# Performance work log

Hardware: AMD Instinct MI355X
Metric: run time of the kernel (lower is better)

## Reference

```python
import jax, jax.numpy as jnp
import numpy as np

B, T, D, H = 8, 1024, 768, 12
HD = D // H  # 64
EPS = 1e-5


def setup_inputs() -> dict:
    key = jax.random.key(0)
    ks = jax.random.split(key, 16)
    s = lambda fan_in: 1.0 / np.sqrt(fan_in)
    inp = {
        "x": jax.random.normal(ks[0], (B, T, D), jnp.float32),
        # per-head Q/K/V projections stacked: [H, D, HD]
        "wq": jax.random.normal(ks[1], (H, D, HD), jnp.float32) * s(D),
        "bq": jnp.zeros((H, HD), jnp.float32),
        "wk": jax.random.normal(ks[2], (H, D, HD), jnp.float32) * s(D),
        "bk": jnp.zeros((H, HD), jnp.float32),
        "wv": jax.random.normal(ks[3], (H, D, HD), jnp.float32) * s(D),
        "bv": jnp.zeros((H, HD), jnp.float32),
        "w_proj": jax.random.normal(ks[4], (D, D), jnp.float32) * s(D),
        "b_proj": jnp.zeros((D,), jnp.float32),
        "g1": jnp.ones((D,), jnp.float32),
        "be1": jnp.zeros((D,), jnp.float32),
        "g2": jnp.ones((D,), jnp.float32),
        "be2": jnp.zeros((D,), jnp.float32),
        "w_fc": jax.random.normal(ks[5], (D, 4 * D), jnp.float32) * s(D),
        "b_fc": jnp.zeros((4 * D,), jnp.float32),
        "w_cp": jax.random.normal(ks[6], (4 * D, D), jnp.float32) * s(4 * D),
        "b_cp": jnp.zeros((D,), jnp.float32),
    }
    return inp


def _layernorm(x, g, b):
    mu = jnp.mean(x, axis=-1, keepdims=True)
    var = jnp.var(x, axis=-1, keepdims=True)
    return (x - mu) * jax.lax.rsqrt(var + EPS) * g + b


def _block(x, wq, bq, wk, bk, wv, bv, w_proj, b_proj, g1, be1, g2, be2,
           w_fc, b_fc, w_cp, b_cp):
    # --- attention sublayer ---
    h = _layernorm(x, g1, be1)
    q = jnp.einsum('btd,hdk->bhtk', h, wq) + bq[None, :, None, :]
    k = jnp.einsum('btd,hdk->bhtk', h, wk) + bk[None, :, None, :]
    v = jnp.einsum('btd,hdk->bhtk', h, wv) + bv[None, :, None, :]
    scale = 1.0 / np.sqrt(HD)
    scores = jnp.einsum('bhqk,bhtk->bhqt', q, k) * scale  # [B,H,T,T]
    causal = jnp.tril(jnp.ones((T, T), bool))
    scores = jnp.where(causal, scores, jnp.finfo(scores.dtype).min)
    attn = jax.nn.softmax(scores, axis=-1)
    y = jnp.einsum('bhqt,bhtk->bhqk', attn, v)           # [B,H,T,HD]
    y = y.transpose(0, 2, 1, 3).reshape(x.shape[0], x.shape[1], D)
    x = x + y @ w_proj + b_proj
    # --- MLP sublayer ---
    h2 = _layernorm(x, g2, be2)
    h2 = jax.nn.gelu(h2 @ w_fc + b_fc, approximate=True)
    return x + h2 @ w_cp + b_cp


def reference(x, wq, bq, wk, bk, wv, bv, w_proj, b_proj, g1, be1, g2, be2,
              w_fc, b_fc, w_cp, b_cp):
    return _block(x, wq, bq, wk, bk, wv, bv, w_proj, b_proj, g1, be1,
                  g2, be2, w_fc, b_fc, w_cp, b_cp)
```

## Files before the change

### kernel.cpp

```cpp
#include <hip/hip_runtime.h>
#include <math.h>


typedef unsigned short ushort_t;
typedef __attribute__((ext_vector_type(8))) __bf16 bf16x8;
typedef __attribute__((ext_vector_type(4))) __bf16 bf16x4;
typedef __attribute__((ext_vector_type(4))) float floatx4;

__device__ __forceinline__ float bf2f(ushort_t u) {
  unsigned int x = ((unsigned int)u) << 16;
  return __builtin_bit_cast(float, x);
}
__device__ __forceinline__ ushort_t f2bf(float f) {
  unsigned int x = __builtin_bit_cast(unsigned int, f);
  unsigned int r = (x + 0x7FFFu + ((x >> 16) & 1u)) >> 16;
  return (ushort_t)r;
}

__global__ void __launch_bounds__(256) transpose_w(const float* __restrict__ in,
                                                   ushort_t* __restrict__ out,
                                                   int R, int C) {
  __shared__ ushort_t tl[64][65];
  int c0 = blockIdx.x * 64, r0 = blockIdx.y * 64;
  #pragma unroll
  for (int i = 0; i < 16; ++i) {
    int idx = threadIdx.x + i * 256;
    int r = idx >> 6, c = idx & 63;
    tl[c][r] = f2bf(in[(size_t)(r0 + r) * C + c0 + c]);
  }
  __syncthreads();
  #pragma unroll
  for (int i = 0; i < 16; ++i) {
    int idx = threadIdx.x + i * 256;
    int c = idx >> 6, r = idx & 63;
    out[(size_t)(c0 + c) * R + r0 + r] = tl[c][r];
  }
}

__global__ void __launch_bounds__(256) repack_qkv_t(const float* __restrict__ wq,
                                                    const float* __restrict__ wk,
                                                    const float* __restrict__ wv,
                                                    ushort_t* __restrict__ out) {
  __shared__ ushort_t tl[64][65];
  int s = blockIdx.y / 12, h = blockIdx.y % 12;
  const float* w = ((s == 0) ? wq : (s == 1) ? wk : wv) + (size_t)h * 768 * 64;
  int d0 = blockIdx.x * 64;
  #pragma unroll
  for (int i = 0; i < 16; ++i) {
    int idx = threadIdx.x + i * 256;
    int r = idx >> 6, c = idx & 63;
    tl[c][r] = f2bf(w[(size_t)(d0 + r) * 64 + c]);
  }
  __syncthreads();
  ushort_t* ob = out + (size_t)(s * 768 + h * 64) * 768;
  #pragma unroll
  for (int i = 0; i < 16; ++i) {
    int idx = threadIdx.x + i * 256;
    int c = idx >> 6, r = idx & 63;
    ob[(size_t)c * 768 + d0 + r] = tl[c][r];
  }
}

__global__ void __launch_bounds__(256) ln_kernel(const float* __restrict__ x,
                                                 const float* __restrict__ g,
                                                 const float* __restrict__ b,
                                                 ushort_t* __restrict__ out) {
  int row = blockIdx.x;
  int tid = threadIdx.x;
  const float* xr = x + (size_t)row * 768;
  float v0 = xr[tid], v1 = xr[tid + 256], v2 = xr[tid + 512];
  float s = v0 + v1 + v2;
  float s2 = v0 * v0 + v1 * v1 + v2 * v2;
  #pragma unroll
  for (int off = 32; off; off >>= 1) {
    s += __shfl_xor(s, off, 64);
    s2 += __shfl_xor(s2, off, 64);
  }
  __shared__ float ws1[4], ws2[4];
  int w = tid >> 6;
  if ((tid & 63) == 0) { ws1[w] = s; ws2[w] = s2; }
  __syncthreads();
  float S = ws1[0] + ws1[1] + ws1[2] + ws1[3];
  float S2 = ws2[0] + ws2[1] + ws2[2] + ws2[3];
  float mean = S * (1.0f / 768.0f);
  float var = S2 * (1.0f / 768.0f) - mean * mean;
  float rstd = rsqrtf(var + 1e-5f);
  ushort_t* orow = out + (size_t)row * 768;
  orow[tid]       = f2bf((v0 - mean) * rstd * g[tid]       + b[tid]);
  orow[tid + 256] = f2bf((v1 - mean) * rstd * g[tid + 256] + b[tid + 256]);
  orow[tid + 512] = f2bf((v2 - mean) * rstd * g[tid + 512] + b[tid + 512]);
}

enum { EPI_QKV = 0, EPI_RES = 1, EPI_FC = 2 };

template <int EPI>
__global__ void __launch_bounds__(256) gemm128(
    const ushort_t* __restrict__ A, const ushort_t* __restrict__ Bt,
    int M, int N, int K,
    const float* __restrict__ b0, const float* __restrict__ b1, const float* __restrict__ b2,
    const float* __restrict__ resid,
    ushort_t* __restrict__ ob0, ushort_t* __restrict__ ob1, ushort_t* __restrict__ ob2,
    float* __restrict__ of) {
  __shared__ __align__(16) ushort_t la[128 * 64];
  __shared__ __align__(16) ushort_t lb[128 * 64];
  int tid = threadIdx.x;
  int lane = tid & 63;
  int w = tid >> 6;
  int wr = w >> 1, wc = w & 1;
  int lm = lane & 15, q = lane >> 4;
  int m0 = blockIdx.x * 128, n0 = blockIdx.y * 128;

  const ushort_t* Ab = A + (size_t)m0 * K;
  const ushort_t* Bb = Bt + (size_t)n0 * K;

  floatx4 acc[4][4];
  #pragma unroll
  for (int i = 0; i < 4; ++i)
    #pragma unroll
    for (int j = 0; j < 4; ++j) acc[i][j] = (floatx4){0.f, 0.f, 0.f, 0.f};

  int srow = tid >> 3;
  int sch  = tid & 7;
  for (int k0 = 0; k0 < K; k0 += 64) {
    uint4 av0 = *reinterpret_cast<const uint4*>(Ab + (size_t)srow * K + k0 + sch * 8);
    uint4 av1 = *reinterpret_cast<const uint4*>(Ab + (size_t)(srow + 32) * K + k0 + sch * 8);
    uint4 av2 = *reinterpret_cast<const uint4*>(Ab + (size_t)(srow + 64) * K + k0 + sch * 8);
    uint4 av3 = *reinterpret_cast<const uint4*>(Ab + (size_t)(srow + 96) * K + k0 + sch * 8);
    uint4 bv0 = *reinterpret_cast<const uint4*>(Bb + (size_t)srow * K + k0 + sch * 8);
    uint4 bv1 = *reinterpret_cast<const uint4*>(Bb + (size_t)(srow + 32) * K + k0 + sch * 8);
    uint4 bv2 = *reinterpret_cast<const uint4*>(Bb + (size_t)(srow + 64) * K + k0 + sch * 8);
    uint4 bv3 = *reinterpret_cast<const uint4*>(Bb + (size_t)(srow + 96) * K + k0 + sch * 8);
    __syncthreads();
    *reinterpret_cast<uint4*>(&la[srow * 64 + ((sch ^ (srow & 7)) << 3)]) = av0;
    *reinterpret_cast<uint4*>(&la[(srow + 32) * 64 + ((sch ^ (srow & 7)) << 3)]) = av1;
    *reinterpret_cast<uint4*>(&la[(srow + 64) * 64 + ((sch ^ (srow & 7)) << 3)]) = av2;
    *reinterpret_cast<uint4*>(&la[(srow + 96) * 64 + ((sch ^ (srow & 7)) << 3)]) = av3;
    *reinterpret_cast<uint4*>(&lb[srow * 64 + ((sch ^ (srow & 7)) << 3)]) = bv0;
    *reinterpret_cast<uint4*>(&lb[(srow + 32) * 64 + ((sch ^ (srow & 7)) << 3)]) = bv1;
    *reinterpret_cast<uint4*>(&lb[(srow + 64) * 64 + ((sch ^ (srow & 7)) << 3)]) = bv2;
    *reinterpret_cast<uint4*>(&lb[(srow + 96) * 64 + ((sch ^ (srow & 7)) << 3)]) = bv3;
    __syncthreads();
    #pragma unroll
    for (int kk = 0; kk < 64; kk += 32) {
      int ch = (kk >> 3) + q;
      bf16x8 af[4], bfr[4];
      #pragma unroll
      for (int i = 0; i < 4; ++i) {
        int ra = wr * 64 + i * 16 + lm;
        int rb = wc * 64 + i * 16 + lm;
        af[i]  = *reinterpret_cast<const bf16x8*>(&la[ra * 64 + ((ch ^ (ra & 7)) << 3)]);
        bfr[i] = *reinterpret_cast<const bf16x8*>(&lb[rb * 64 + ((ch ^ (rb & 7)) << 3)]);
      }
      #pragma unroll
      for (int i = 0; i < 4; ++i)
        #pragma unroll
        for (int j = 0; j < 4; ++j)
          acc[i][j] = __builtin_amdgcn_mfma_f32_16x16x32_bf16(af[i], bfr[j], acc[i][j], 0, 0, 0);
    }
  }

  #pragma unroll
  for (int i = 0; i < 4; ++i) {
    #pragma unroll
    for (int j = 0; j < 4; ++j) {
      #pragma unroll
      for (int r = 0; r < 4; ++r) {
        float vacc = acc[i][j][r];
        int mm = m0 + wr * 64 + i * 16 + q * 4 + r;
        int nn = n0 + wc * 64 + j * 16 + lm;
        if constexpr (EPI == EPI_QKV) {
          int sel = nn / 768;
          int nq = nn - sel * 768;
          const float* bp = (sel == 0) ? b0 : (sel == 1) ? b1 : b2;
          ushort_t* dst = (sel == 0) ? ob0 : (sel == 1) ? ob1 : ob2;
          int bh = (mm >> 10) * 12 + (nq >> 6);
          size_t o = (size_t)bh * 65536 + (size_t)(mm & 1023) * 64 + (nq & 63);
          dst[o] = f2bf(vacc + bp[nq]);
        } else if constexpr (EPI == EPI_RES) {
          size_t o = (size_t)mm * 768 + nn;
          of[o] = vacc + b0[nn] + resid[o];
        } else {
          float u = vacc + b0[nn];
          float inner = 0.7978845608028654f * (u + 0.044715f * u * u * u);
          float gl = 0.5f * u * (1.0f + tanhf(inner));
          ob0[(size_t)mm * 3072 + nn] = f2bf(gl);
        }
      }
    }
  }
}

__global__ void __launch_bounds__(256) transpose_v(const ushort_t* __restrict__ vb,
                                                   ushort_t* __restrict__ vt) {
  __shared__ ushort_t tl[64 * 72];
  int kt = blockIdx.x, bh = blockIdx.y;
  size_t base = (size_t)bh * 65536;
  int tid = threadIdx.x;
  #pragma unroll
  for (int i = 0; i < 2; ++i) {
    int r = (tid >> 3) + i * 32;
    int cb = (tid & 7) * 8;
    *reinterpret_cast<uint4*>(&tl[r * 72 + cb]) =
        *reinterpret_cast<const uint4*>(vb + base + (size_t)(kt * 64 + r) * 64 + cb);
  }
  __syncthreads();
  #pragma unroll
  for (int i = 0; i < 2; ++i) {
    int dim = (tid >> 3) + i * 32;
    int kb8 = (tid & 7) * 8;
    ushort_t tmp[8];
    #pragma unroll
    for (int j = 0; j < 8; ++j) tmp[j] = tl[(kb8 + j) * 72 + dim];
    *reinterpret_cast<uint4*>(vt + base + (size_t)dim * 1024 + kt * 64 + kb8) =
        *reinterpret_cast<uint4*>(tmp);
  }
}

__global__ void __launch_bounds__(256) attn_mfma(const ushort_t* __restrict__ qb,
                                                 const ushort_t* __restrict__ kb,
                                                 const ushort_t* __restrict__ vtb,
                                                 ushort_t* __restrict__ yb) {
  __shared__ __align__(16) ushort_t kl[64 * 72];
  __shared__ __align__(16) ushort_t vtl[64 * 72];
  int qt = (int)gridDim.x - 1 - (int)blockIdx.x;
  int bh = blockIdx.y;
  int tid = threadIdx.x, lane = tid & 63, w = tid >> 6;
  int col = lane & 15, quad = lane >> 4;
  int qw0 = qt * 64 + w * 16;
  size_t base = (size_t)bh * 65536;

  bf16x8 qf0 = *reinterpret_cast<const bf16x8*>(qb + base + (size_t)(qw0 + col) * 64 + quad * 8);
  bf16x8 qf1 = *reinterpret_cast<const bf16x8*>(qb + base + (size_t)(qw0 + col) * 64 + 32 + quad * 8);

  floatx4 O[4];
  #pragma unroll
  for (int ss = 0; ss < 4; ++ss) O[ss] = (floatx4){0.f, 0.f, 0.f, 0.f};
  float m = -INFINITY, l = 0.f;
  const float sscale = 0.125f * 1.4426950408889634f;
  int qg = qw0 + col;

  for (int kt0 = 0; kt0 <= qt * 64; kt0 += 64) {
    __syncthreads();
    #pragma unroll
    for (int i = 0; i < 2; ++i) {
      int r = (tid >> 3) + i * 32;
      int cb = (tid & 7) * 8;
      *reinterpret_cast<uint4*>(&kl[r * 72 + cb]) =
          *reinterpret_cast<const uint4*>(kb + base + (size_t)(kt0 + r) * 64 + cb);
      *reinterpret_cast<uint4*>(&vtl[r * 72 + cb]) =
          *reinterpret_cast<const uint4*>(vtb + base + (size_t)r * 1024 + kt0 + cb);
    }
    __syncthreads();
    int nk = qw0 + 16 - kt0;
    if (nk > 64) nk = 64;
    int ng = (nk + 31) >> 5;
    for (int g = 0; g < ng; ++g) {
      int ksA = kt0 + g * 32;
      int ksB = ksA + 16;
      int rbase = (g * 32 + col) * 72;
      bf16x8 kfA0 = *reinterpret_cast<const bf16x8*>(&kl[rbase + quad * 8]);
      bf16x8 kfA1 = *reinterpret_cast<const bf16x8*>(&kl[rbase + 32 + quad * 8]);
      bf16x8 kfB0 = *reinterpret_cast<const bf16x8*>(&kl[rbase + 16 * 72 + quad * 8]);
      bf16x8 kfB1 = *reinterpret_cast<const bf16x8*>(&kl[rbase + 16 * 72 + 32 + quad * 8]);
      floatx4 saA = (floatx4){0.f, 0.f, 0.f, 0.f};
      floatx4 saB = (floatx4){0.f, 0.f, 0.f, 0.f};
      __builtin_amdgcn_s_setprio(1);
      saA = __builtin_amdgcn_mfma_f32_16x16x32_bf16(kfA0, qf0, saA, 0, 0, 0);
      saA = __builtin_amdgcn_mfma_f32_16x16x32_bf16(kfA1, qf1, saA, 0, 0, 0);
      saB = __builtin_amdgcn_mfma_f32_16x16x32_bf16(kfB0, qf0, saB, 0, 0, 0);
      saB = __builtin_amdgcn_mfma_f32_16x16x32_bf16(kfB1, qf1, saB, 0, 0, 0);
      __builtin_amdgcn_s_setprio(0);
      float s0 = saA[0] * sscale, s1 = saA[1] * sscale;
      float s2 = saA[2] * sscale, s3 = saA[3] * sscale;
      float s4 = saB[0] * sscale, s5 = saB[1] * sscale;
      float s6 = saB[2] * sscale, s7 = saB[3] * sscale;
      if (ksA + 15 > qw0) {
        int keyb = ksA + quad * 4;
        if (keyb + 0 > qg) s0 = -3.0e38f;
        if (keyb + 1 > qg) s1 = -3.0e38f;
        if (keyb + 2 > qg) s2 = -3.0e38f;
        if (keyb + 3 > qg) s3 = -3.0e38f;
      }
      if (ksB + 15 > qw0) {
        int keyb = ksB + quad * 4;
        if (keyb + 0 > qg) s4 = -3.0e38f;
        if (keyb + 1 > qg) s5 = -3.0e38f;
        if (keyb + 2 > qg) s6 = -3.0e38f;
        if (keyb + 3 > qg) s7 = -3.0e38f;
      }
      float mloc = fmaxf(fmaxf(fmaxf(s0, s1), fmaxf(s2, s3)),
                         fmaxf(fmaxf(s4, s5), fmaxf(s6, s7)));
      mloc = fmaxf(mloc, __shfl_xor(mloc, 16, 64));
      mloc = fmaxf(mloc, __shfl_xor(mloc, 32, 64));
      float mnew = fmaxf(m, mloc);
      float c = __builtin_amdgcn_exp2f(m - mnew);
      float p0 = __builtin_amdgcn_exp2f(s0 - mnew);
      float p1 = __builtin_amdgcn_exp2f(s1 - mnew);
      float p2 = __builtin_amdgcn_exp2f(s2 - mnew);
      float p3 = __builtin_amdgcn_exp2f(s3 - mnew);
      float p4 = __builtin_amdgcn_exp2f(s4 - mnew);
      float p5 = __builtin_amdgcn_exp2f(s5 - mnew);
      float p6 = __builtin_amdgcn_exp2f(s6 - mnew);
      float p7 = __builtin_amdgcn_exp2f(s7 - mnew);
      float ll = ((p0 + p1) + (p2 + p3)) + ((p4 + p5) + (p6 + p7));
      ll += __shfl_xor(ll, 16, 64);
      ll += __shfl_xor(ll, 32, 64);
      l = l * c + ll;
      m = mnew;
      float c0 = __shfl(c, quad * 4 + 0, 64);
      float c1 = __shfl(c, quad * 4 + 1, 64);
      float c2 = __shfl(c, quad * 4 + 2, 64);
      float c3 = __shfl(c, quad * 4 + 3, 64);
      bf16x8 pf = {(__bf16)p0, (__bf16)p1, (__bf16)p2, (__bf16)p3,
                   (__bf16)p4, (__bf16)p5, (__bf16)p6, (__bf16)p7};
      __builtin_amdgcn_s_setprio(1);
      #pragma unroll
      for (int ss = 0; ss < 4; ++ss) {
        O[ss][0] *= c0; O[ss][1] *= c1; O[ss][2] *= c2; O[ss][3] *= c3;
        int vrow = (ss * 16 + col) * 72 + g * 32 + quad * 4;
        bf16x4 va = *reinterpret_cast<const bf16x4*>(&vtl[vrow]);
        bf16x4 vb = *reinterpret_cast<const bf16x4*>(&vtl[vrow + 16]);
        bf16x8 vf = {va[0], va[1], va[2], va[3], vb[0], vb[1], vb[2], vb[3]};
        O[ss] = __builtin_amdgcn_mfma_f32_16x16x32_bf16(pf, vf, O[ss], 0, 0, 0);
      }
      __builtin_amdgcn_s_setprio(0);
    }
  }
  float linv = 1.0f / l;
  float l0 = __shfl(linv, quad * 4 + 0, 64);
  float l1 = __shfl(linv, quad * 4 + 1, 64);
  float l2 = __shfl(linv, quad * 4 + 2, 64);
  float l3 = __shfl(linv, quad * 4 + 3, 64);
  int b = bh / 12, h = bh - b * 12;
  #pragma unroll
  for (int ss = 0; ss < 4; ++ss) {
    float lr[4] = {l0, l1, l2, l3};
    #pragma unroll
    for (int r = 0; r < 4; ++r) {
      int t = qw0 + quad * 4 + r;
      yb[((size_t)(b * 1024 + t)) * 768 + h * 64 + ss * 16 + col] = f2bf(O[ss][r] * lr[r]);
    }
  }
}

extern "C" void kernel_launch(void* const* d_in, const int* in_sizes, int n_in,
                              void* d_out, int out_size, void* d_ws, size_t ws_size,
                              hipStream_t stream) {
  const float* x      = (const float*)d_in[0];
  const float* wq     = (const float*)d_in[1];
  const float* bq     = (const float*)d_in[2];
  const float* wk     = (const float*)d_in[3];
  const float* bk     = (const float*)d_in[4];
  const float* wv     = (const float*)d_in[5];
  const float* bv     = (const float*)d_in[6];
  const float* w_proj = (const float*)d_in[7];
  const float* b_proj = (const float*)d_in[8];
  const float* g1     = (const float*)d_in[9];
  const float* be1    = (const float*)d_in[10];
  const float* g2     = (const float*)d_in[11];
  const float* be2    = (const float*)d_in[12];
  const float* w_fc   = (const float*)d_in[13];
  const float* b_fc   = (const float*)d_in[14];
  const float* w_cp   = (const float*)d_in[15];
  const float* b_cp   = (const float*)d_in[16];
  float* out = (float*)d_out;

  char* ws = (char*)d_ws;
  size_t off = 0;
  auto alloc = [&](size_t bytes) -> char* {
    char* p = ws + off;
    off += (bytes + 255) & ~(size_t)255;
    return p;
  };
  const size_t MD = 8192ull * 768;
  ushort_t* wqkvT  = (ushort_t*)alloc(2304ull * 768 * 2);
  ushort_t* wprojT = (ushort_t*)alloc(768ull * 768 * 2);
  ushort_t* wfcT   = (ushort_t*)alloc(3072ull * 768 * 2);
  ushort_t* wcpT   = (ushort_t*)alloc(768ull * 3072 * 2);
  ushort_t* hbuf   = (ushort_t*)alloc(MD * 2);
  ushort_t* qbuf   = (ushort_t*)alloc(MD * 2);
  ushort_t* kbuf   = (ushort_t*)alloc(MD * 2);
  ushort_t* vbuf   = (ushort_t*)alloc(MD * 2);
  ushort_t* ybuf   = (ushort_t*)alloc(MD * 2);
  float*    x1     = (float*)alloc(MD * 4);
  ushort_t* h2buf  = (ushort_t*)alloc(MD * 2);
  ushort_t* vtbuf  = hbuf;
  ushort_t* fcbuf  = qbuf;

  repack_qkv_t<<<dim3(12, 36), 256, 0, stream>>>(wq, wk, wv, wqkvT);
  transpose_w<<<dim3(12, 12), 256, 0, stream>>>(w_proj, wprojT, 768, 768);
  transpose_w<<<dim3(48, 12), 256, 0, stream>>>(w_fc, wfcT, 768, 3072);
  transpose_w<<<dim3(12, 48), 256, 0, stream>>>(w_cp, wcpT, 3072, 768);

  ln_kernel<<<8192, 256, 0, stream>>>(x, g1, be1, hbuf);
  gemm128<EPI_QKV><<<dim3(64, 18), 256, 0, stream>>>(
      hbuf, wqkvT, 8192, 2304, 768, bq, bk, bv, nullptr, qbuf, kbuf, vbuf, nullptr);
  transpose_v<<<dim3(16, 96), 256, 0, stream>>>(vbuf, vtbuf);
  attn_mfma<<<dim3(16, 96), 256, 0, stream>>>(qbuf, kbuf, vtbuf, ybuf);
  gemm128<EPI_RES><<<dim3(64, 6), 256, 0, stream>>>(
      ybuf, wprojT, 8192, 768, 768, b_proj, nullptr, nullptr, x,
      nullptr, nullptr, nullptr, x1);
  ln_kernel<<<8192, 256, 0, stream>>>(x1, g2, be2, h2buf);
  gemm128<EPI_FC><<<dim3(64, 24), 256, 0, stream>>>(
      h2buf, wfcT, 8192, 3072, 768, b_fc, nullptr, nullptr, nullptr,
      fcbuf, nullptr, nullptr, nullptr);
  gemm128<EPI_RES><<<dim3(64, 6), 256, 0, stream>>>(
      fcbuf, wcpT, 8192, 768, 3072, b_cp, nullptr, nullptr, x1,
      nullptr, nullptr, nullptr, out);
}
```

Baseline: 441.6 us.

## Load K/V fragments directly from global memory and split causal diagonal tile

Removes the shared-memory staging of K and V^T tiles and the two block barriers per key tile in the attention kernel. Each wave now loads its MFMA operands straight from global memory, relying on the cache for reuse across the four waves. Off-diagonal tiles are processed as full 64-key blocks with no masking, and only the diagonal tile keeps the masked 32-key loop. This trades LDS traffic and synchronisation for redundant global and cache loads with less coalesced V accesses.

After: 602.2 us. 36.4% more time.

```diff
diff --git a/kernel.cpp b/kernel.cpp
--- a/kernel.cpp
+++ b/kernel.cpp
@@ -220,14 +220,14 @@
                                                  const ushort_t* __restrict__ kb,
                                                  const ushort_t* __restrict__ vtb,
                                                  ushort_t* __restrict__ yb) {
-  __shared__ __align__(16) ushort_t kl[64 * 72];
-  __shared__ __align__(16) ushort_t vtl[64 * 72];
   int qt = (int)gridDim.x - 1 - (int)blockIdx.x;
   int bh = blockIdx.y;
   int tid = threadIdx.x, lane = tid & 63, w = tid >> 6;
   int col = lane & 15, quad = lane >> 4;
   int qw0 = qt * 64 + w * 16;
   size_t base = (size_t)bh * 65536;
+  const ushort_t* kbb = kb + base;
+  const ushort_t* vtbb = vtb + base;
 
   bf16x8 qf0 = *reinterpret_cast<const bf16x8*>(qb + base + (size_t)(qw0 + col) * 64 + quad * 8);
   bf16x8 qf1 = *reinterpret_cast<const bf16x8*>(qb + base + (size_t)(qw0 + col) * 64 + 32 + quad * 8);
@@ -237,31 +237,95 @@
   for (int ss = 0; ss < 4; ++ss) O[ss] = (floatx4){0.f, 0.f, 0.f, 0.f};
   float m = -INFINITY, l = 0.f;
   const float sscale = 0.125f * 1.4426950408889634f;
-  int qg = qw0 + col;
-
-  for (int kt0 = 0; kt0 <= qt * 64; kt0 += 64) {
-    __syncthreads();
-    #pragma unroll
-    for (int i = 0; i < 2; ++i) {
-      int r = (tid >> 3) + i * 32;
-      int cb = (tid & 7) * 8;
-      *reinterpret_cast<uint4*>(&kl[r * 72 + cb]) =
-          *reinterpret_cast<const uint4*>(kb + base + (size_t)(kt0 + r) * 64 + cb);
-      *reinterpret_cast<uint4*>(&vtl[r * 72 + cb]) =
-          *reinterpret_cast<const uint4*>(vtb + base + (size_t)r * 1024 + kt0 + cb);
+
+  for (int kt0 = 0; kt0 < qt * 64; kt0 += 64) {
+    const ushort_t* kp = kbb + (size_t)(kt0 + col) * 64 + quad * 8;
+    bf16x8 kA0 = *reinterpret_cast<const bf16x8*>(kp);
+    bf16x8 kA1 = *reinterpret_cast<const bf16x8*>(kp + 32);
+    bf16x8 kB0 = *reinterpret_cast<const bf16x8*>(kp + 1024);
+    bf16x8 kB1 = *reinterpret_cast<const bf16x8*>(kp + 1056);
+    bf16x8 kC0 = *reinterpret_cast<const bf16x8*>(kp + 2048);
+    bf16x8 kC1 = *reinterpret_cast<const bf16x8*>(kp + 2080);
+    bf16x8 kD0 = *reinterpret_cast<const bf16x8*>(kp + 3072);
+    bf16x8 kD1 = *reinterpret_cast<const bf16x8*>(kp + 3104);
+    floatx4 sA = (floatx4){0.f, 0.f, 0.f, 0.f};
+    floatx4 sB = (floatx4){0.f, 0.f, 0.f, 0.f};
+    floatx4 sC = (floatx4){0.f, 0.f, 0.f, 0.f};
+    floatx4 sD = (floatx4){0.f, 0.f, 0.f, 0.f};
+    __builtin_amdgcn_s_setprio(1);
+    sA = __builtin_amdgcn_mfma_f32_16x16x32_bf16(kA0, qf0, sA, 0, 0, 0);
+    sA = __builtin_amdgcn_mfma_f32_16x16x32_bf16(kA1, qf1, sA, 0, 0, 0);
+    sB = __builtin_amdgcn_mfma_f32_16x16x32_bf16(kB0, qf0, sB, 0, 0, 0);
+    sB = __builtin_amdgcn_mfma_f32_16x16x32_bf16(kB1, qf1, sB, 0, 0, 0);
+    sC = __builtin_amdgcn_mfma_f32_16x16x32_bf16(kC0, qf0, sC, 0, 0, 0);
+    sC = __builtin_amdgcn_mfma_f32_16x16x32_bf16(kC1, qf1, sC, 0, 0, 0);
+    sD = __builtin_amdgcn_mfma_f32_16x16x32_bf16(kD0, qf0, sD, 0, 0, 0);
+    sD = __builtin_amdgcn_mfma_f32_16x16x32_bf16(kD1, qf1, sD, 0, 0, 0);
+    __builtin_amdgcn_s_setprio(0);
+    float t0 = sA[0] * sscale, t1 = sA[1] * sscale, t2 = sA[2] * sscale, t3 = sA[3] * sscale;
+    float t4 = sB[0] * sscale, t5 = sB[1] * sscale, t6 = sB[2] * sscale, t7 = sB[3] * sscale;
+    float t8 = sC[0] * sscale, t9 = sC[1] * sscale, tA = sC[2] * sscale, tB = sC[3] * sscale;
+    float tC = sD[0] * sscale, tD = sD[1] * sscale, tE = sD[2] * sscale, tF = sD[3] * sscale;
+    float mloc = fmaxf(fmaxf(fmaxf(fmaxf(t0, t1), fmaxf(t2, t3)),
+                             fmaxf(fmaxf(t4, t5), fmaxf(t6, t7))),
+                       fmaxf(fmaxf(fmaxf(t8, t9), fmaxf(tA, tB)),
+                             fmaxf(fmaxf(tC, tD), fmaxf(tE, tF))));
+    mloc = fmaxf(mloc, __shfl_xor(mloc, 16, 64));
+    mloc = fmaxf(mloc, __shfl_xor(mloc, 32, 64));
+    float mnew = fmaxf(m, mloc);
+    float c = __builtin_amdgcn_exp2f(m - mnew);
+    float p0 = __builtin_amdgcn_exp2f(t0 - mnew), p1 = __builtin_amdgcn_exp2f(t1 - mnew);
+    float p2 = __builtin_amdgcn_exp2f(t2 - mnew), p3 = __builtin_amdgcn_exp2f(t3 - mnew);
+    float p4 = __builtin_amdgcn_exp2f(t4 - mnew), p5 = __builtin_amdgcn_exp2f(t5 - mnew);
+    float p6 = __builtin_amdgcn_exp2f(t6 - mnew), p7 = __builtin_amdgcn_exp2f(t7 - mnew);
+    float p8 = __builtin_amdgcn_exp2f(t8 - mnew), p9 = __builtin_amdgcn_exp2f(t9 - mnew);
+    float pA = __builtin_amdgcn_exp2f(tA - mnew), pB = __builtin_amdgcn_exp2f(tB - mnew);
+    float pC = __builtin_amdgcn_exp2f(tC - mnew), pD = __builtin_amdgcn_exp2f(tD - mnew);
+    float pE = __builtin_amdgcn_exp2f(tE - mnew), pF = __builtin_amdgcn_exp2f(tF - mnew);
+    float ll = (((p0 + p1) + (p2 + p3)) + ((p4 + p5) + (p6 + p7))) +
+               (((p8 + p9) + (pA + pB)) + ((pC + pD) + (pE + pF)));
+    ll += __shfl_xor(ll, 16, 64);
+    ll += __shfl_xor(ll, 32, 64);
+    l = l * c + ll;
+    m = mnew;
+    float c0 = __shfl(c, quad * 4 + 0, 64);
+    float c1 = __shfl(c, quad * 4 + 1, 64);
+    float c2 = __shfl(c, quad * 4 + 2, 64);
+    float c3 = __shfl(c, quad * 4 + 3, 64);
+    bf16x8 pfA = {(__bf16)p0, (__bf16)p1, (__bf16)p2, (__bf16)p3,
+                  (__bf16)p4, (__bf16)p5, (__bf16)p6, (__bf16)p7};
+    bf16x8 pfB = {(__bf16)p8, (__bf16)p9, (__bf16)pA, (__bf16)pB,
+                  (__bf16)pC, (__bf16)pD, (__bf16)pE, (__bf16)pF};
+    __builtin_amdgcn_s_setprio(1);
+    #pragma unroll
+    for (int ss = 0; ss < 4; ++ss) {
+      O[ss][0] *= c0; O[ss][1] *= c1; O[ss][2] *= c2; O[ss][3] *= c3;
+      const ushort_t* vp = vtbb + (size_t)(ss * 16 + col) * 1024 + kt0 + quad * 4;
+      bf16x4 va = *reinterpret_cast<const bf16x4*>(vp);
+      bf16x4 vb = *reinterpret_cast<const bf16x4*>(vp + 16);
+      bf16x4 vc = *reinterpret_cast<const bf16x4*>(vp + 32);
+      bf16x4 vd = *reinterpret_cast<const bf16x4*>(vp + 48);
+      bf16x8 vfA = {va[0], va[1], va[2], va[3], vb[0], vb[1], vb[2], vb[3]};
+      bf16x8 vfB = {vc[0], vc[1], vc[2], vc[3], vd[0], vd[1], vd[2], vd[3]};
+      O[ss] = __builtin_amdgcn_mfma_f32_16x16x32_bf16(pfA, vfA, O[ss], 0, 0, 0);
+      O[ss] = __builtin_amdgcn_mfma_f32_16x16x32_bf16(pfB, vfB, O[ss], 0, 0, 0);
     }
-    __syncthreads();
-    int nk = qw0 + 16 - kt0;
-    if (nk > 64) nk = 64;
+    __builtin_amdgcn_s_setprio(0);
+  }
+
+  {
+    int kt0 = qt * 64;
+    int qg = qw0 + col;
+    int nk = w * 16 + 16;
     int ng = (nk + 31) >> 5;
     for (int g = 0; g < ng; ++g) {
       int ksA = kt0 + g * 32;
       int ksB = ksA + 16;
-      int rbase = (g * 32 + col) * 72;
-      bf16x8 kfA0 = *reinterpret_cast<const bf16x8*>(&kl[rbase + quad * 8]);
-      bf16x8 kfA1 = *reinterpret_cast<const bf16x8*>(&kl[rbase + 32 + quad * 8]);
-      bf16x8 kfB0 = *reinterpret_cast<const bf16x8*>(&kl[rbase + 16 * 72 + quad * 8]);
-      bf16x8 kfB1 = *reinterpret_cast<const bf16x8*>(&kl[rbase + 16 * 72 + 32 + quad * 8]);
+      const ushort_t* kp = kbb + (size_t)(ksA + col) * 64 + quad * 8;
+      bf16x8 kfA0 = *reinterpret_cast<const bf16x8*>(kp);
+      bf16x8 kfA1 = *reinterpret_cast<const bf16x8*>(kp + 32);
+      bf16x8 kfB0 = *reinterpret_cast<const bf16x8*>(kp + 1024);
+      bf16x8 kfB1 = *reinterpret_cast<const bf16x8*>(kp + 1056);
       floatx4 saA = (floatx4){0.f, 0.f, 0.f, 0.f};
       floatx4 saB = (floatx4){0.f, 0.f, 0.f, 0.f};
       __builtin_amdgcn_s_setprio(1);
@@ -317,15 +381,16 @@
       #pragma unroll
       for (int ss = 0; ss < 4; ++ss) {
         O[ss][0] *= c0; O[ss][1] *= c1; O[ss][2] *= c2; O[ss][3] *= c3;
-        int vrow = (ss * 16 + col) * 72 + g * 32 + quad * 4;
-        bf16x4 va = *reinterpret_cast<const bf16x4*>(&vtl[vrow]);
-        bf16x4 vb = *reinterpret_cast<const bf16x4*>(&vtl[vrow + 16]);
+        const ushort_t* vp = vtbb + (size_t)(ss * 16 + col) * 1024 + kt0 + g * 32 + quad * 4;
+        bf16x4 va = *reinterpret_cast<const bf16x4*>(vp);
+        bf16x4 vb = *reinterpret_cast<const bf16x4*>(vp + 16);
         bf16x8 vf = {va[0], va[1], va[2], va[3], vb[0], vb[1], vb[2], vb[3]};
         O[ss] = __builtin_amdgcn_mfma_f32_16x16x32_bf16(pf, vf, O[ss], 0, 0, 0);
       }
       __builtin_amdgcn_s_setprio(0);
     }
   }
+
   float linv = 1.0f / l;
   float l0 = __shfl(linv, quad * 4 + 0, 64);
   float l1 = __shfl(linv, quad * 4 + 1, 64);
```
